# Optimization experiments

Measured on AMD Instinct MI355X. Metric: run time of the kernel, lower is better.

Reference implementation:

```python
import jax, jax.numpy as jnp
import numpy as np

BINS = 10
LOSS_WEIGHT = 1.0
EDGE_TOP = 1.0 + 1e-6  # edges[-1] += 1e-6 in the torch module


def setup_inputs() -> dict:
    key = jax.random.key(0)
    k1, k2, k3 = jax.random.split(key, 3)
    shape = (32, 1048576)
    # pred: sigmoid probabilities in [0, 1)
    pred = jax.random.uniform(k1, shape, dtype=jnp.float32)
    target = (jax.random.uniform(k2, shape) < 0.3).astype(jnp.float32)
    label_weight = (jax.random.uniform(k3, shape) < 0.95).astype(jnp.float32)
    return {"pred": pred, "target": target, "label_weight": label_weight}


def reference(pred, target, label_weight):
    p = pred.reshape(-1)
    t = target.reshape(-1).astype(p.dtype)
    lw = label_weight.reshape(-1).astype(p.dtype)

    I = jnp.sum(p * t)                       # intersection
    S = jnp.sum(p) + jnp.sum(t)              # denominator of Dice

    # gradient norm proxy: |2I/S * pred.detach() - target| (no grad flows through g)
    g = jax.lax.stop_gradient(jnp.abs(2.0 * I / S * p - t))

    valid = lw > 0
    tot = jnp.maximum(jnp.sum(valid.astype(p.dtype)), 1.0)

    # bin assignment: edges are i/bins for i=0..bins, with edges[-1] bumped by 1e-6,
    # so g in [i/bins, (i+1)/bins) -> bin i, and g in [1, 1+1e-6) -> bin bins-1.
    in_range = valid & (g < EDGE_TOP)
    bin_idx = jnp.clip(jnp.floor(g * BINS).astype(jnp.int32), 0, BINS - 1)

    # one-pass histogram of valid, in-range elements
    counts = jnp.zeros(BINS, dtype=p.dtype).at[bin_idx].add(in_range.astype(p.dtype))
    n_nonempty = jnp.sum(counts > 0).astype(p.dtype)

    # weight = tot / num_in_bin for elements in a non-empty bin, else 0; then /n
    per_elem = jnp.where(in_range, tot / jnp.maximum(counts[bin_idx], 1.0), 0.0)
    weights = per_elem / jnp.maximum(n_nonempty, 1.0)

    loss = 1.0 - jnp.sum(2.0 * p * t * weights) / S
    return loss * LOSS_WEIGHT
```

## Files before the change

kernel.cpp:

```cpp
#include <hip/hip_runtime.h>


constexpr int BINS   = 10;
constexpr int K      = 4;
constexpr int CH     = 256 * K;
constexpr int BLOCKS = 2048;
constexpr int OFF1   = 64;
constexpr int OFF2   = 16448;
constexpr size_t MASK_OFF = 266240;

#define SB0 __builtin_amdgcn_sched_barrier(0)

__device__ __forceinline__ void acc3(const float4& pv, const float4& tv,
                                     float& sI, float& sP, float& sT) {
    sI += pv.x * tv.x + pv.y * tv.y + pv.z * tv.z + pv.w * tv.w;
    sP += pv.x + pv.y + pv.z + pv.w;
    sT += tv.x + tv.y + tv.z + tv.w;
}

__device__ __forceinline__ unsigned mbyte(const float4& tv, const float4& wv) {
    unsigned mb = 0;
    mb |= (tv.x != 0.f) ? 1u   : 0u;  mb |= (tv.y != 0.f) ? 2u   : 0u;
    mb |= (tv.z != 0.f) ? 4u   : 0u;  mb |= (tv.w != 0.f) ? 8u   : 0u;
    mb |= (wv.x != 0.f) ? 16u  : 0u;  mb |= (wv.y != 0.f) ? 32u  : 0u;
    mb |= (wv.z != 0.f) ? 64u  : 0u;  mb |= (wv.w != 0.f) ? 128u : 0u;
    return mb;
}

template<bool MASK>
__global__ __launch_bounds__(256) void k_pass1(const float4* __restrict__ p,
                                               const float4* __restrict__ t,
                                               const float4* __restrict__ lw,
                                               unsigned* __restrict__ maskw,
                                               float* __restrict__ ws,
                                               int n4, int n) {
    const int tid   = threadIdx.x;
    const int nfull = n4 / CH;
    const int G     = gridDim.x;
    float sI = 0.f, sP = 0.f, sT = 0.f;

    if constexpr (MASK) {
        float4 Ap[K], At[K], Aw[K], Bp[K], Bt[K], Bw[K];

#define P1_LOAD(P_, T_, W_, c) do { \
        const int _b = (c) * CH + tid; \
        _Pragma("unroll") for (int k = 0; k < K; ++k) P_[k] = p[_b + k * 256]; \
        _Pragma("unroll") for (int k = 0; k < K; ++k) T_[k] = t[_b + k * 256]; \
        _Pragma("unroll") for (int k = 0; k < K; ++k) W_[k] = lw[_b + k * 256]; \
    } while (0)

#define P1_CONS(P_, T_, W_, c) do { \
        _Pragma("unroll") for (int k = 0; k < K; ++k) acc3(P_[k], T_[k], sI, sP, sT); \
        unsigned mw = mbyte(T_[0], W_[0]) | (mbyte(T_[1], W_[1]) << 8) | \
                      (mbyte(T_[2], W_[2]) << 16) | (mbyte(T_[3], W_[3]) << 24); \
        maskw[(c) * 256 + tid] = mw; \
    } while (0)

        const int bid   = blockIdx.x;
        const int count = (bid < nfull) ? (nfull - 1 - bid) / G + 1 : 0;
        if (count > 0) {
            P1_LOAD(Ap, At, Aw, bid);
            int j = 0;
            for (; j + 2 <= count; j += 2) {
                P1_LOAD(Bp, Bt, Bw, bid + (j + 1) * G);
                SB0;
                P1_CONS(Ap, At, Aw, bid + j * G);
                if (j + 2 < count) P1_LOAD(Ap, At, Aw, bid + (j + 2) * G);
                SB0;
                P1_CONS(Bp, Bt, Bw, bid + (j + 1) * G);
            }
            if (count & 1) {
                SB0;
                P1_CONS(Ap, At, Aw, bid + (count - 1) * G);
            }
        }
#undef P1_LOAD
#undef P1_CONS
    } else {
        for (int c = blockIdx.x; c < nfull; c += G) {
            const int base = c * CH + tid;
            float4 pv[K], tv[K];
#pragma unroll
            for (int k = 0; k < K; ++k) pv[k] = p[base + k * 256];
#pragma unroll
            for (int k = 0; k < K; ++k) tv[k] = t[base + k * 256];
#pragma unroll
            for (int k = 0; k < K; ++k) acc3(pv[k], tv[k], sI, sP, sT);
        }
    }

    if (blockIdx.x == 0) {
        for (int i = nfull * CH + tid; i < n4; i += 256) {
            float4 pv = p[i], tv = t[i];
            acc3(pv, tv, sI, sP, sT);
        }
        if (tid == 0) {
            const float* pf = (const float*)p;
            const float* tf = (const float*)t;
            for (int i = n4 * 4; i < n; ++i) { sI += pf[i] * tf[i]; sP += pf[i]; sT += tf[i]; }
        }
    }
#pragma unroll
    for (int o = 32; o > 0; o >>= 1) {
        sI += __shfl_down(sI, o);
        sP += __shfl_down(sP, o);
        sT += __shfl_down(sT, o);
    }
    __shared__ float rI[4], rP[4], rT[4];
    int wave = tid >> 6, lane = tid & 63;
    if (lane == 0) { rI[wave] = sI; rP[wave] = sP; rT[wave] = sT; }
    __syncthreads();
    if (tid == 0) {
        float* o = &ws[OFF1 + blockIdx.x * 4];
        o[0] = rI[0] + rI[1] + rI[2] + rI[3];
        o[1] = rP[0] + rP[1] + rP[2] + rP[3];
        o[2] = rT[0] + rT[1] + rT[2] + rT[3];
    }
}

__global__ __launch_bounds__(256) void k_mid(float* __restrict__ ws, int nb1) {
    const float4* pws = (const float4*)&ws[OFF1];
    float aI = 0.f, aP = 0.f, aT = 0.f;
    for (int b = threadIdx.x; b < nb1; b += 256) {
        float4 v = pws[b];
        aI += v.x; aP += v.y; aT += v.z;
    }
    __shared__ float red[256 * 5];
    float* mine = &red[threadIdx.x * 5];
    mine[0] = aI; mine[1] = aP; mine[2] = aT;
    __syncthreads();
    int tid = threadIdx.x;
    if (tid < 3) {
        float s = 0.f;
        for (int i = 0; i < 256; ++i) s += red[i * 5 + tid];
        red[tid] = s;
    }
    __syncthreads();
    if (tid == 0) {
        float I = red[0];
        float S = red[1] + red[2];
        ws[0] = 2.f * I / S;
        ws[1] = S;
    }
}

template<bool MASK>
__global__ __launch_bounds__(256) void k_pass2(const float4* __restrict__ p,
                                               const float4* __restrict__ t,
                                               const float4* __restrict__ lw,
                                               const unsigned* __restrict__ maskw,
                                               float* __restrict__ ws,
                                               int n4, int n) {
    const float scale    = ws[0];
    const float edge_top = 1.0f + 1e-6f;
    const int tid   = threadIdx.x;
    const int nfull = n4 / CH;
    const int G     = gridDim.x;

    int   cnt[BINS];
    float sm[BINS];
#pragma unroll
    for (int b = 0; b < BINS; ++b) { cnt[b] = 0; sm[b] = 0.f; }
    int vcount = 0;

    auto process = [&](float pe, float te, bool valid) {
        vcount += valid;
        float g = fabsf(scale * pe - te);
        bool inr = valid && (g < edge_top);
        int b = (int)(g * 10.f);
        b = b > (BINS - 1) ? (BINS - 1) : b;
        int slot = inr ? b : BINS;
        float adds = 2.f * pe * te;
#pragma unroll
        for (int b0 = 0; b0 < BINS; ++b0) {
            bool m = (slot == b0);
            cnt[b0] += m;
            sm[b0]  += m ? adds : 0.f;
        }
    };
    auto procq = [&](const float4& q, unsigned b) {
        process(q.x, (b & 1u) ? 1.f : 0.f, (b & 16u)  != 0);
        process(q.y, (b & 2u) ? 1.f : 0.f, (b & 32u)  != 0);
        process(q.z, (b & 4u) ? 1.f : 0.f, (b & 64u)  != 0);
        process(q.w, (b & 8u) ? 1.f : 0.f, (b & 128u) != 0);
    };

    if constexpr (MASK) {
        float4 Ap[K], Bp[K];
        unsigned Am, Bm;

#define P2_LOAD(P_, M_, c) do { \
        const int _b = (c) * CH + tid; \
        _Pragma("unroll") for (int k = 0; k < K; ++k) P_[k] = p[_b + k * 256]; \
        M_ = maskw[(c) * 256 + tid]; \
    } while (0)

#define P2_CONS(P_, M_) do { \
        procq(P_[0], M_);        procq(P_[1], M_ >> 8); \
        procq(P_[2], M_ >> 16);  procq(P_[3], M_ >> 24); \
    } while (0)

        const int bid   = blockIdx.x;
        const int count = (bid < nfull) ? (nfull - 1 - bid) / G + 1 : 0;
        if (count > 0) {
            P2_LOAD(Ap, Am, bid);
            int j = 0;
            for (; j + 2 <= count; j += 2) {
                P2_LOAD(Bp, Bm, bid + (j + 1) * G);
                SB0;
                P2_CONS(Ap, Am);
                if (j + 2 < count) P2_LOAD(Ap, Am, bid + (j + 2) * G);
                SB0;
                P2_CONS(Bp, Bm);
            }
            if (count & 1) {
                SB0;
                P2_CONS(Ap, Am);
            }
        }
#undef P2_LOAD
#undef P2_CONS
    } else {
        for (int c = blockIdx.x; c < nfull; c += G) {
            const int base = c * CH + tid;
            float4 pv[K], tv[K], wv[K];
#pragma unroll
            for (int k = 0; k < K; ++k) pv[k] = p[base + k * 256];
#pragma unroll
            for (int k = 0; k < K; ++k) tv[k] = t[base + k * 256];
#pragma unroll
            for (int k = 0; k < K; ++k) wv[k] = lw[base + k * 256];
#pragma unroll
            for (int k = 0; k < K; ++k) {
                process(pv[k].x, tv[k].x, wv[k].x > 0.f);
                process(pv[k].y, tv[k].y, wv[k].y > 0.f);
                process(pv[k].z, tv[k].z, wv[k].z > 0.f);
                process(pv[k].w, tv[k].w, wv[k].w > 0.f);
            }
        }
    }

    if (blockIdx.x == 0) {
        for (int i = nfull * CH + tid; i < n4; i += 256) {
            float4 pv = p[i], tv = t[i], wv = lw[i];
            process(pv.x, tv.x, wv.x > 0.f);
            process(pv.y, tv.y, wv.y > 0.f);
            process(pv.z, tv.z, wv.z > 0.f);
            process(pv.w, tv.w, wv.w > 0.f);
        }
        if (tid == 0) {
            const float* pf = (const float*)p;
            const float* tf = (const float*)t;
            const float* wf = (const float*)lw;
            for (int i = n4 * 4; i < n; ++i) process(pf[i], tf[i], wf[i] > 0.f);
        }
    }

    __shared__ float red[256 * 21];
    float* mine = &red[tid * 21];
#pragma unroll
    for (int b0 = 0; b0 < BINS; ++b0) {
        mine[b0]        = (float)cnt[b0];
        mine[BINS + b0] = sm[b0];
    }
    mine[2 * BINS] = (float)vcount;
    __syncthreads();

    if (tid < 2 * BINS + 1) {
        float v = 0.f;
        for (int i = 0; i < 256; ++i) v += red[i * 21 + tid];
        ws[OFF2 + blockIdx.x * 24 + tid] = v;
    }
}

__global__ __launch_bounds__(256) void k_final(const float* __restrict__ ws,
                                               float* __restrict__ out, int nb2) {
    float acc[24];
#pragma unroll
    for (int s = 0; s < 24; ++s) acc[s] = 0.f;

    for (int b = threadIdx.x; b < nb2; b += 256) {
        const float4* rec = (const float4*)&ws[OFF2 + b * 24];
        float4 v0 = rec[0], v1 = rec[1], v2 = rec[2],
               v3 = rec[3], v4 = rec[4], v5 = rec[5];
        acc[0]  += v0.x; acc[1]  += v0.y; acc[2]  += v0.z; acc[3]  += v0.w;
        acc[4]  += v1.x; acc[5]  += v1.y; acc[6]  += v1.z; acc[7]  += v1.w;
        acc[8]  += v2.x; acc[9]  += v2.y; acc[10] += v2.z; acc[11] += v2.w;
        acc[12] += v3.x; acc[13] += v3.y; acc[14] += v3.z; acc[15] += v3.w;
        acc[16] += v4.x; acc[17] += v4.y; acc[18] += v4.z; acc[19] += v4.w;
        acc[20] += v5.x;
    }

    __shared__ float red[256 * 25];
    float* mine = &red[threadIdx.x * 25];
#pragma unroll
    for (int s = 0; s <= 2 * BINS; ++s) mine[s] = acc[s];
    __syncthreads();

    __shared__ float fin[24];
    int tid = threadIdx.x;
    if (tid <= 2 * BINS) {
        float s = 0.f;
        for (int i = 0; i < 256; ++i) s += red[i * 25 + tid];
        fin[tid] = s;
    }
    __syncthreads();
    if (tid == 0) {
        float S   = ws[1];
        float tot = fmaxf(fin[20], 1.0f);
        int nne = 0;
        for (int b = 0; b < BINS; ++b) nne += (fin[b] > 0.f) ? 1 : 0;
        float nn = fmaxf((float)nne, 1.0f);
        float wsum = 0.f;
        for (int b = 0; b < BINS; ++b) {
            float c = fmaxf(fin[b], 1.0f);
            wsum += fin[BINS + b] * (tot / c);
        }
        wsum /= nn;
        out[0] = 1.0f - wsum / S;
    }
}

extern "C" void kernel_launch(void* const* d_in, const int* in_sizes, int n_in,
                              void* d_out, int out_size, void* d_ws, size_t ws_size,
                              hipStream_t stream) {
    const float* p  = (const float*)d_in[0];
    const float* t  = (const float*)d_in[1];
    const float* lw = (const float*)d_in[2];
    float* ws  = (float*)d_ws;
    float* out = (float*)d_out;
    int n  = in_sizes[0];
    int n4 = n >> 2;

    unsigned* maskw = (unsigned*)((char*)d_ws + MASK_OFF);
    const bool use_mask = ws_size >= MASK_OFF + (size_t)n4;

    if (use_mask) {
        k_pass1<true><<<BLOCKS, 256, 0, stream>>>((const float4*)p, (const float4*)t,
                                                  (const float4*)lw, maskw, ws, n4, n);
        k_mid<<<1, 256, 0, stream>>>(ws, BLOCKS);
        k_pass2<true><<<BLOCKS, 256, 0, stream>>>((const float4*)p, (const float4*)t,
                                                  (const float4*)lw, maskw, ws, n4, n);
        k_final<<<1, 256, 0, stream>>>(ws, out, BLOCKS);
    } else {
        k_pass1<false><<<BLOCKS, 256, 0, stream>>>((const float4*)p, (const float4*)t,
                                                   (const float4*)lw, maskw, ws, n4, n);
        k_mid<<<1, 256, 0, stream>>>(ws, BLOCKS);
        k_pass2<false><<<BLOCKS, 256, 0, stream>>>((const float4*)p, (const float4*)t,
                                                   (const float4*)lw, maskw, ws, n4, n);
        k_final<<<1, 256, 0, stream>>>(ws, out, BLOCKS);
    }
}
```

Measured before the change: 406.5 us.

## Split input into four quarter streams and drop manual double-buffered pipelining

Each thread now reads one float4 from each of four widely separated quarters of the input instead of four consecutive 256-float4 slices, and the mask word indexing follows that quarter layout. The hand-written A/B register double buffering with sched_barriers is removed in favour of a plain grid-stride loop, leaving load scheduling to the compiler. The aim is simpler code with fewer live registers and possibly better occupancy, at the risk of losing the explicit load/compute overlap and of spreading accesses over four distant DRAM streams.

```diff
diff --git a/kernel.cpp b/kernel.cpp
--- a/kernel.cpp
+++ b/kernel.cpp
@@ -2,14 +2,10 @@
 
 
 constexpr int BINS   = 10;
-constexpr int K      = 4;
-constexpr int CH     = 256 * K;
 constexpr int BLOCKS = 2048;
 constexpr int OFF1   = 64;
 constexpr int OFF2   = 16448;
 constexpr size_t MASK_OFF = 266240;
-
-#define SB0 __builtin_amdgcn_sched_barrier(0)
 
 __device__ __forceinline__ void acc3(const float4& pv, const float4& tv,
                                      float& sI, float& sP, float& sT) {
@@ -34,63 +30,45 @@
                                                unsigned* __restrict__ maskw,
                                                float* __restrict__ ws,
                                                int n4, int n) {
-    const int tid   = threadIdx.x;
-    const int nfull = n4 / CH;
-    const int G     = gridDim.x;
+    const int tid    = threadIdx.x;
+    const int G      = gridDim.x;
+    const int nq     = n4 >> 2;
+    const int nfullq = nq >> 8;
     float sI = 0.f, sP = 0.f, sT = 0.f;
 
     if constexpr (MASK) {
-        float4 Ap[K], At[K], Aw[K], Bp[K], Bt[K], Bw[K];
-
-#define P1_LOAD(P_, T_, W_, c) do { \
-        const int _b = (c) * CH + tid; \
-        _Pragma("unroll") for (int k = 0; k < K; ++k) P_[k] = p[_b + k * 256]; \
-        _Pragma("unroll") for (int k = 0; k < K; ++k) T_[k] = t[_b + k * 256]; \
-        _Pragma("unroll") for (int k = 0; k < K; ++k) W_[k] = lw[_b + k * 256]; \
-    } while (0)
-
-#define P1_CONS(P_, T_, W_, c) do { \
-        _Pragma("unroll") for (int k = 0; k < K; ++k) acc3(P_[k], T_[k], sI, sP, sT); \
-        unsigned mw = mbyte(T_[0], W_[0]) | (mbyte(T_[1], W_[1]) << 8) | \
-                      (mbyte(T_[2], W_[2]) << 16) | (mbyte(T_[3], W_[3]) << 24); \
-        maskw[(c) * 256 + tid] = mw; \
-    } while (0)
-
-        const int bid   = blockIdx.x;
-        const int count = (bid < nfull) ? (nfull - 1 - bid) / G + 1 : 0;
-        if (count > 0) {
-            P1_LOAD(Ap, At, Aw, bid);
-            int j = 0;
-            for (; j + 2 <= count; j += 2) {
-                P1_LOAD(Bp, Bt, Bw, bid + (j + 1) * G);
-                SB0;
-                P1_CONS(Ap, At, Aw, bid + j * G);
-                if (j + 2 < count) P1_LOAD(Ap, At, Aw, bid + (j + 2) * G);
-                SB0;
-                P1_CONS(Bp, Bt, Bw, bid + (j + 1) * G);
+        for (int c = blockIdx.x; c < nfullq; c += G) {
+            const int b0 = c * 256 + tid;
+            float4 p0 = p[b0], p1 = p[b0 + nq], p2 = p[b0 + 2 * nq], p3 = p[b0 + 3 * nq];
+            float4 t0 = t[b0], t1 = t[b0 + nq], t2 = t[b0 + 2 * nq], t3 = t[b0 + 3 * nq];
+            float4 w0 = lw[b0], w1 = lw[b0 + nq], w2 = lw[b0 + 2 * nq], w3 = lw[b0 + 3 * nq];
+            acc3(p0, t0, sI, sP, sT);
+            acc3(p1, t1, sI, sP, sT);
+            acc3(p2, t2, sI, sP, sT);
+            acc3(p3, t3, sI, sP, sT);
+            unsigned mw = mbyte(t0, w0) | (mbyte(t1, w1) << 8) |
+                          (mbyte(t2, w2) << 16) | (mbyte(t3, w3) << 24);
+            maskw[b0] = mw;
+        }
+    } else {
+        for (int c = blockIdx.x; c < nfullq; c += G) {
+            const int b0 = c * 256 + tid;
+            float4 p0 = p[b0], p1 = p[b0 + nq], p2 = p[b0 + 2 * nq], p3 = p[b0 + 3 * nq];
+            float4 t0 = t[b0], t1 = t[b0 + nq], t2 = t[b0 + 2 * nq], t3 = t[b0 + 3 * nq];
+            acc3(p0, t0, sI, sP, sT);
+            acc3(p1, t1, sI, sP, sT);
+            acc3(p2, t2, sI, sP, sT);
+            acc3(p3, t3, sI, sP, sT);
+        }
+    }
+
+    if (blockIdx.x == 0) {
+        for (int q = 0; q < 4; ++q)
+            for (int i = q * nq + nfullq * 256 + tid; i < (q + 1) * nq; i += 256) {
+                float4 pv = p[i], tv = t[i];
+                acc3(pv, tv, sI, sP, sT);
             }
-            if (count & 1) {
-                SB0;
-                P1_CONS(Ap, At, Aw, bid + (count - 1) * G);
-            }
-        }
-#undef P1_LOAD
-#undef P1_CONS
-    } else {
-        for (int c = blockIdx.x; c < nfull; c += G) {
-            const int base = c * CH + tid;
-            float4 pv[K], tv[K];
-#pragma unroll
-            for (int k = 0; k < K; ++k) pv[k] = p[base + k * 256];
-#pragma unroll
-            for (int k = 0; k < K; ++k) tv[k] = t[base + k * 256];
-#pragma unroll
-            for (int k = 0; k < K; ++k) acc3(pv[k], tv[k], sI, sP, sT);
-        }
-    }
-
-    if (blockIdx.x == 0) {
-        for (int i = nfull * CH + tid; i < n4; i += 256) {
+        for (int i = 4 * nq + tid; i < n4; i += 256) {
             float4 pv = p[i], tv = t[i];
             acc3(pv, tv, sI, sP, sT);
         }
@@ -153,9 +131,10 @@
                                                int n4, int n) {
     const float scale    = ws[0];
     const float edge_top = 1.0f + 1e-6f;
-    const int tid   = threadIdx.x;
-    const int nfull = n4 / CH;
-    const int G     = gridDim.x;
+    const int tid    = threadIdx.x;
+    const int G      = gridDim.x;
+    const int nq     = n4 >> 2;
+    const int nfullq = nq >> 8;
 
     int   cnt[BINS];
     float sm[BINS];
@@ -186,62 +165,39 @@
     };
 
     if constexpr (MASK) {
-        float4 Ap[K], Bp[K];
-        unsigned Am, Bm;
-
-#define P2_LOAD(P_, M_, c) do { \
-        const int _b = (c) * CH + tid; \
-        _Pragma("unroll") for (int k = 0; k < K; ++k) P_[k] = p[_b + k * 256]; \
-        M_ = maskw[(c) * 256 + tid]; \
-    } while (0)
-
-#define P2_CONS(P_, M_) do { \
-        procq(P_[0], M_);        procq(P_[1], M_ >> 8); \
-        procq(P_[2], M_ >> 16);  procq(P_[3], M_ >> 24); \
-    } while (0)
-
-        const int bid   = blockIdx.x;
-        const int count = (bid < nfull) ? (nfull - 1 - bid) / G + 1 : 0;
-        if (count > 0) {
-            P2_LOAD(Ap, Am, bid);
-            int j = 0;
-            for (; j + 2 <= count; j += 2) {
-                P2_LOAD(Bp, Bm, bid + (j + 1) * G);
-                SB0;
-                P2_CONS(Ap, Am);
-                if (j + 2 < count) P2_LOAD(Ap, Am, bid + (j + 2) * G);
-                SB0;
-                P2_CONS(Bp, Bm);
+        for (int c = blockIdx.x; c < nfullq; c += G) {
+            const int b0 = c * 256 + tid;
+            float4 p0 = p[b0], p1 = p[b0 + nq], p2 = p[b0 + 2 * nq], p3 = p[b0 + 3 * nq];
+            unsigned mw = maskw[b0];
+            procq(p0, mw);
+            procq(p1, mw >> 8);
+            procq(p2, mw >> 16);
+            procq(p3, mw >> 24);
+        }
+    } else {
+        for (int c = blockIdx.x; c < nfullq; c += G) {
+            const int b0 = c * 256 + tid;
+#pragma unroll
+            for (int q = 0; q < 4; ++q) {
+                float4 pv = p[b0 + q * nq], tv = t[b0 + q * nq], wv = lw[b0 + q * nq];
+                process(pv.x, tv.x, wv.x > 0.f);
+                process(pv.y, tv.y, wv.y > 0.f);
+                process(pv.z, tv.z, wv.z > 0.f);
+                process(pv.w, tv.w, wv.w > 0.f);
             }
-            if (count & 1) {
-                SB0;
-                P2_CONS(Ap, Am);
+        }
+    }
+
+    if (blockIdx.x == 0) {
+        for (int q = 0; q < 4; ++q)
+            for (int i = q * nq + nfullq * 256 + tid; i < (q + 1) * nq; i += 256) {
+                float4 pv = p[i], tv = t[i], wv = lw[i];
+                process(pv.x, tv.x, wv.x > 0.f);
+                process(pv.y, tv.y, wv.y > 0.f);
+                process(pv.z, tv.z, wv.z > 0.f);
+                process(pv.w, tv.w, wv.w > 0.f);
             }
-        }
-#undef P2_LOAD
-#undef P2_CONS
-    } else {
-        for (int c = blockIdx.x; c < nfull; c += G) {
-            const int base = c * CH + tid;
-            float4 pv[K], tv[K], wv[K];
-#pragma unroll
-            for (int k = 0; k < K; ++k) pv[k] = p[base + k * 256];
-#pragma unroll
-            for (int k = 0; k < K; ++k) tv[k] = t[base + k * 256];
-#pragma unroll
-            for (int k = 0; k < K; ++k) wv[k] = lw[base + k * 256];
-#pragma unroll
-            for (int k = 0; k < K; ++k) {
-                process(pv[k].x, tv[k].x, wv[k].x > 0.f);
-                process(pv[k].y, tv[k].y, wv[k].y > 0.f);
-                process(pv[k].z, tv[k].z, wv[k].z > 0.f);
-                process(pv[k].w, tv[k].w, wv[k].w > 0.f);
-            }
-        }
-    }
-
-    if (blockIdx.x == 0) {
-        for (int i = nfull * CH + tid; i < n4; i += 256) {
+        for (int i = 4 * nq + tid; i < n4; i += 256) {
             float4 pv = p[i], tv = t[i], wv = lw[i];
             process(pv.x, tv.x, wv.x > 0.f);
             process(pv.y, tv.y, wv.y > 0.f);
```

Result: no change. 413.0 us (+1.6%).
